# Performance work log

Hardware: AMD Instinct MI355X
Metric: run time of the kernel (lower is better)

## Reference

```python
import jax, jax.numpy as jnp
import numpy as np

N_HEAD = 16


def setup_inputs() -> dict:
    key = jax.random.key(0)
    k1, k2, k3 = jax.random.split(key, 3)
    B, S, D = 2, 2048, 1024
    return {
        "hidden_states": jax.random.normal(k1, (B, S, D), dtype=jnp.float32),
        "c_attn_w": jax.random.normal(k2, (D, 3 * D), dtype=jnp.float32) * 0.02,
        "c_attn_b": jnp.zeros((3 * D,), dtype=jnp.float32),
        "c_proj_w": jax.random.normal(k3, (D, D), dtype=jnp.float32) * 0.02,
        "c_proj_b": jnp.zeros((D,), dtype=jnp.float32),
    }


def reference(hidden_states, c_attn_w, c_attn_b, c_proj_w, c_proj_b):
    B, S, D = hidden_states.shape
    H = N_HEAD
    hd = D // H
    # Fused QKV projection (Conv1D == linear with transposed weight layout)
    qkv = hidden_states @ c_attn_w + c_attn_b  # [B,S,3D]
    q, k, v = jnp.split(qkv, 3, axis=-1)
    # split heads -> [B,H,S,hd]
    q = q.reshape(B, S, H, hd).transpose(0, 2, 1, 3)
    k = k.reshape(B, S, H, hd).transpose(0, 2, 1, 3)
    v = v.reshape(B, S, H, hd).transpose(0, 2, 1, 3)
    # scaled dot-product with causal mask
    scores = jnp.einsum("bhqd,bhkd->bhqk", q, k) / jnp.asarray(hd ** 0.5, q.dtype)
    causal = jnp.tril(jnp.ones((S, S), dtype=bool))  # [S,S]
    mask_value = jnp.finfo(scores.dtype).min
    scores = jnp.where(causal[None, None, :, :], scores, mask_value)
    attn_weights = jax.nn.softmax(scores, axis=-1)  # [B,H,S,S]
    ctx = jnp.einsum("bhqk,bhkd->bhqd", attn_weights, v)  # [B,H,S,hd]
    ctx = ctx.transpose(0, 2, 1, 3).reshape(B, S, D)  # merge heads
    out = ctx @ c_proj_w + c_proj_b  # [B,S,D]
    return out
```

## Files before the change

kernel.cpp:

```cpp
#include <hip/hip_runtime.h>
#include <hip/hip_bf16.h>

typedef __attribute__((ext_vector_type(8))) short short8;
typedef __attribute__((ext_vector_type(4))) float f32x4;
typedef __attribute__((ext_vector_type(16))) float f32x16;
typedef __attribute__((ext_vector_type(4))) unsigned short u16x4;
typedef __attribute__((ext_vector_type(8))) unsigned short u16x8;
typedef __attribute__((ext_vector_type(4))) unsigned int u32x4;

#define MFMA16(a, b, c) __builtin_amdgcn_mfma_f32_16x16x32_bf16((a), (b), (c), 0, 0, 0)
#define MFMA32(a, b, c) __builtin_amdgcn_mfma_f32_32x32x16_bf16((a), (b), (c), 0, 0, 0)

__device__ __forceinline__ unsigned short f2bf(float f) {
    union { float f; unsigned u; } v; v.f = f;
    return (unsigned short)((v.u + 0x7fffu + ((v.u >> 16) & 1u)) >> 16);
}

__device__ __forceinline__ float bf2f(unsigned short s) {
    union { unsigned u; float f; } v; v.u = (unsigned)s << 16;
    return v.f;
}

__device__ __forceinline__ unsigned cvtpk(float lo, float hi_) {
    unsigned r;
    asm volatile("v_cvt_pk_bf16_f32 %0, %1, %2" : "=v"(r) : "v"(lo), "v"(hi_));
    return r;
}

__global__ void cast_x_kernel(const float* __restrict__ x, ushort* __restrict__ y) {
    int i = blockIdx.x * blockDim.x + threadIdx.x;
    float4 v = ((const float4*)x)[i];
    u16x4 o = { f2bf(v.x), f2bf(v.y), f2bf(v.z), f2bf(v.w) };
    *(u16x4*)(y + (size_t)i * 4) = o;
}

__global__ void transpose_cast_kernel(const float* __restrict__ W, ushort* __restrict__ WT,
                                      int K, int N) {
    __shared__ ushort t[64][66];
    int n0 = blockIdx.x * 64, k0 = blockIdx.y * 64;
    int tn = threadIdx.x & 63, tg = threadIdx.x >> 6;
#pragma unroll
    for (int i = 0; i < 16; ++i) {
        int k = tg * 16 + i;
        t[tn][k] = f2bf(W[(size_t)(k0 + k) * N + n0 + tn]);
    }
    __syncthreads();
#pragma unroll
    for (int i = 0; i < 16; ++i) {
        int nn = tg * 16 + i;
        WT[(size_t)(n0 + nn) * K + k0 + tn] = t[nn][tn];
    }
}

#define QSCALE 0.18033688011112042f

template <int MODE>
__global__ __launch_bounds__(256, 3)
void gemm_bt_kernel(const ushort* __restrict__ A, const ushort* __restrict__ BT,
                    const float* __restrict__ bias,
                    ushort* __restrict__ Qb, ushort* __restrict__ Kb,
                    ushort* __restrict__ VT, float* __restrict__ Out,
                    int M, int N, int K) {
    __shared__ ushort Asm[3][128 * 32];
    __shared__ ushort Bsm[3][128 * 32];
    const int tid = threadIdx.x;
    const int lane = tid & 63;
    const int wv = tid >> 6;
    const int l15 = lane & 15, lg = lane >> 4;
    const int rm = (wv >> 1) * 64, cn = (wv & 1) * 64;
    const int row0 = blockIdx.y * 128, col0 = blockIdx.x * 128;

    const char* Agb = (const char*)(A + (size_t)row0 * K);
    const char* Bgb = (const char*)(BT + (size_t)col0 * K);
    const size_t rowbytes = (size_t)K * 2;

    f32x4 acc[4][4];
#pragma unroll
    for (int mi = 0; mi < 4; ++mi)
#pragma unroll
        for (int ni = 0; ni < 4; ++ni) acc[mi][ni] = f32x4{0.f, 0.f, 0.f, 0.f};

    const int sr0 = tid >> 2, sc0 = (tid & 3) ^ (sr0 & 3);
    const int sr1 = (tid + 256) >> 2, sc1 = (tid & 3) ^ (sr1 & 3);

#define GSTAGE(buf, k0_)                                                                \
    do {                                                                                \
        size_t kbyte = (size_t)(k0_)*2;                                                 \
        __builtin_amdgcn_global_load_lds(                                               \
            (const __attribute__((address_space(1))) void*)(Agb + (size_t)sr0 *         \
                rowbytes + kbyte + sc0 * 16),                                           \
            (__attribute__((address_space(3))) void*)((char*)&Asm[buf][0] + tid * 16),  \
            16, 0, 0);                                                                  \
        __builtin_amdgcn_global_load_lds(                                               \
            (const __attribute__((address_space(1))) void*)(Agb + (size_t)sr1 *         \
                rowbytes + kbyte + sc1 * 16),                                           \
            (__attribute__((address_space(3))) void*)((char*)&Asm[buf][0] + 4096 +      \
                tid * 16),                                                              \
            16, 0, 0);                                                                  \
        __builtin_amdgcn_global_load_lds(                                               \
            (const __attribute__((address_space(1))) void*)(Bgb + (size_t)sr0 *         \
                rowbytes + kbyte + sc0 * 16),                                           \
            (__attribute__((address_space(3))) void*)((char*)&Bsm[buf][0] + tid * 16),  \
            16, 0, 0);                                                                  \
        __builtin_amdgcn_global_load_lds(                                               \
            (const __attribute__((address_space(1))) void*)(Bgb + (size_t)sr1 *         \
                rowbytes + kbyte + sc1 * 16),                                           \
            (__attribute__((address_space(3))) void*)((char*)&Bsm[buf][0] + 4096 +      \
                tid * 16),                                                              \
            16, 0, 0);                                                                  \
    } while (0)

    const int NK = K >> 5;
    GSTAGE(0, 0);
    GSTAGE(1, 32);

    const int sw8 = (lg ^ (l15 & 3)) << 3;

    int cur = 0, stg = 2;
    for (int i = 0; i < NK; ++i) {
        if (i < NK - 1) asm volatile("s_waitcnt vmcnt(4)" ::: "memory");
        else            asm volatile("s_waitcnt vmcnt(0)" ::: "memory");
        __builtin_amdgcn_s_barrier();
        if (i + 2 < NK) GSTAGE(stg, (i + 2) * 32);
        short8 af[4], bf[4];
#pragma unroll
        for (int mi = 0; mi < 4; ++mi)
            af[mi] = *(const short8*)&Asm[cur][(rm + mi * 16 + l15) * 32 + sw8];
#pragma unroll
        for (int ni = 0; ni < 4; ++ni)
            bf[ni] = *(const short8*)&Bsm[cur][(cn + ni * 16 + l15) * 32 + sw8];
        __builtin_amdgcn_s_setprio(1);
#pragma unroll
        for (int mi = 0; mi < 4; ++mi)
#pragma unroll
            for (int ni = 0; ni < 4; ++ni)
                acc[mi][ni] = MFMA16(af[mi], bf[ni], acc[mi][ni]);
        __builtin_amdgcn_s_setprio(0);
        cur = (cur == 2) ? 0 : cur + 1;
        stg = (stg == 2) ? 0 : stg + 1;
    }
#undef GSTAGE

    if (MODE == 0) {
        const int sect = col0 >> 10;
#pragma unroll
        for (int ni = 0; ni < 4; ++ni) {
            int col = col0 + cn + ni * 16 + l15;
            float bv = bias[col];
            int dcol = col & 1023, h = dcol >> 6, dd = dcol & 63;
#pragma unroll
            for (int mi = 0; mi < 4; ++mi) {
                int mrow0 = row0 + rm + mi * 16 + lg * 4;
                if (sect == 2) {
                    int b = mrow0 >> 11, s = mrow0 & 2047;
                    u16x4 o;
#pragma unroll
                    for (int j = 0; j < 4; ++j) o[j] = f2bf(acc[mi][ni][j] + bv);
                    *(u16x4*)&VT[((size_t)((b << 4) + h) * 64 + dd) * 2048 + s] = o;
                } else {
                    ushort* dst = sect ? Kb : Qb;
                    float sc = sect ? 1.f : QSCALE;
#pragma unroll
                    for (int j = 0; j < 4; ++j) {
                        int tok = mrow0 + j;
                        int b = tok >> 11, s = tok & 2047;
                        dst[((size_t)((b << 4) + h) * 2048 + s) * 64 + dd] =
                            f2bf((acc[mi][ni][j] + bv) * sc);
                    }
                }
            }
        }
    } else {
#pragma unroll
        for (int ni = 0; ni < 4; ++ni) {
            int col = col0 + cn + ni * 16 + l15;
            float bv = bias[col];
#pragma unroll
            for (int mi = 0; mi < 4; ++mi) {
                int mrow0 = row0 + rm + mi * 16 + lg * 4;
#pragma unroll
                for (int j = 0; j < 4; ++j)
                    Out[(size_t)(mrow0 + j) * N + col] = acc[mi][ni][j] + bv;
            }
        }
    }
}

template <int SPLIT>
__global__ __launch_bounds__(256, 4)
void attn_kernel(const ushort* __restrict__ Qb, const ushort* __restrict__ Kb,
                 const ushort* __restrict__ VT, ushort* __restrict__ CTX,
                 ushort* __restrict__ OP, float* __restrict__ ML) {
    __shared__ __align__(16) ushort Ksm[2][64 * 64];
    __shared__ __align__(16) ushort Vsm[2][64 * 64];

    const int tid = threadIdx.x;
    const int lane = tid & 63;
    const int w = tid >> 6;
    const int l31 = lane & 31;
    const int hi = lane >> 5;
    const int r7 = l31 & 7;

    const int id = blockIdx.x;
    int bh, qt, half, cBeg, cEnd;
    if (SPLIT) {
        const int xcd = id & 7, jj = id >> 3;
        bh = (xcd << 2) + (jj & 3);
        const int r = jj >> 2;
        half = r >> 4;
        const int s = r & 15;
        qt = (s < 8) ? s : 23 - s;
        cBeg = half * (qt + 1);
        cEnd = cBeg + (qt + 1);
    } else {
        const int xcd = id & 7, jj = id >> 3;
        bh = (xcd << 2) + (jj >> 4);
        qt = ((jj >> 5) & 1) ? (jj & 15) : 15 - (jj & 15);
        half = 0; cBeg = 0; cEnd = 2 * qt + 2;
    }
    const int nc = 2 * qt + 2;
    const int qw0 = qt * 128 + w * 32;
    const int qrow = qw0 + l31;

    const ushort* Qh = Qb + (size_t)bh * 2048 * 64;
    const ushort* Kh = Kb + (size_t)bh * 2048 * 64;
    const ushort* Vh = VT + (size_t)bh * 64 * 2048;

    short8 qf[4];
#pragma unroll
    for (int dc = 0; dc < 4; ++dc)
        qf[dc] = *(const short8*)&Qh[(size_t)qrow * 64 + dc * 16 + hi * 8];

    const int srow = tid >> 3;
    const int sxor = ((tid & 7) ^ (srow & 7)) * 8;

#define GLL(src, dst) __builtin_amdgcn_global_load_lds(                                 \
        (const __attribute__((address_space(1))) void*)(src),                           \
        (__attribute__((address_space(3))) void*)(dst), 16, 0, 0)

#define STAGE(buf, kb_)                                                                 \
    do {                                                                                \
        const ushort* kp = Kh + (size_t)((kb_) + srow) * 64 + sxor;                     \
        GLL(kp, (char*)&Ksm[buf][0] + tid * 16);                                        \
        GLL(kp + 32 * 64, (char*)&Ksm[buf][0] + 4096 + tid * 16);                       \
        const ushort* vp = Vh + (size_t)srow * 2048 + (kb_) + sxor;                     \
        GLL(vp, (char*)&Vsm[buf][0] + tid * 16);                                        \
        GLL(vp + (size_t)32 * 2048, (char*)&Vsm[buf][0] + 4096 + tid * 16);             \
    } while (0)

    const int cdiag = 2 * qt + (w >> 1);

    STAGE(0, cBeg * 64);
    __syncthreads();

    float mrun = -1e30f, lsum = 0.f;
    f32x16 acc0, acc1;
#pragma unroll
    for (int r = 0; r < 16; ++r) { acc0[r] = 0.f; acc1[r] = 0.f; }

    int cur = 0;
    for (int c = cBeg; c < cEnd; ++c) {
        const int kb = c * 64;
        if (c + 1 < cEnd) STAGE(cur ^ 1, kb + 64);

        if (!(w < 2 && c == nc - 1)) {
            const ushort* Kc = &Ksm[cur][0];
            const ushort* Vc = &Vsm[cur][0];

            f32x16 st0, st1;
#pragma unroll
            for (int r = 0; r < 16; ++r) { st0[r] = 0.f; st1[r] = 0.f; }
            __builtin_amdgcn_s_setprio(1);
#pragma unroll
            for (int dc = 0; dc < 4; ++dc) {
                short8 kf0 = *(const short8*)(Kc + l31 * 64 + (((dc * 2 + hi) ^ r7) << 3));
                short8 kf1 = *(const short8*)(Kc + (32 + l31) * 64 + (((dc * 2 + hi) ^ r7) << 3));
                st0 = MFMA32(kf0, qf[dc], st0);
                st1 = MFMA32(kf1, qf[dc], st1);
            }
            __builtin_amdgcn_s_setprio(0);

            if (c == cdiag) {
                const int base0 = kb + (hi << 2);
                const int base1 = kb + 32 + (hi << 2);
#pragma unroll
                for (int r = 0; r < 16; ++r) {
                    int k0 = base0 + ((r & 3) + 8 * (r >> 2));
                    int k1 = base1 + ((r & 3) + 8 * (r >> 2));
                    st0[r] = (k0 <= qrow) ? st0[r] : -1e30f;
                    st1[r] = (k1 <= qrow) ? st1[r] : -1e30f;
                }
            }

            float tm[8];
#pragma unroll
            for (int i = 0; i < 8; ++i)
                tm[i] = fmaxf(fmaxf(st0[i], st0[i + 8]), fmaxf(st1[i], st1[i + 8]));
            float tmax = fmaxf(fmaxf(fmaxf(tm[0], tm[1]), fmaxf(tm[2], tm[3])),
                               fmaxf(fmaxf(tm[4], tm[5]), fmaxf(tm[6], tm[7])));
            tmax = fmaxf(tmax, __shfl_xor(tmax, 32));

            if (!__all(tmax <= mrun + 8.0f)) {
                float mnew = fmaxf(mrun, tmax);
                float sc = exp2f(mrun - mnew);
#pragma unroll
                for (int r = 0; r < 16; ++r) { acc0[r] *= sc; acc1[r] *= sc; }
                lsum *= sc;
                mrun = mnew;
            }

#pragma unroll
            for (int r = 0; r < 16; ++r) st0[r] = exp2f(st0[r] - mrun);
#pragma unroll
            for (int r = 0; r < 16; ++r) st1[r] = exp2f(st1[r] - mrun);
            float ts[8];
#pragma unroll
            for (int i = 0; i < 8; ++i) ts[i] = st0[i] + st0[i + 8];
#pragma unroll
            for (int i = 0; i < 8; ++i) ts[i] += st1[i] + st1[i + 8];
            float tsum = ((ts[0] + ts[1]) + (ts[2] + ts[3])) +
                         ((ts[4] + ts[5]) + (ts[6] + ts[7]));
            lsum += tsum;

#define MAKE_PFRAG(st, kcL, out)                                                        \
    do {                                                                                \
        unsigned a0 = cvtpk(st[8 * kcL + 0], st[8 * kcL + 1]);                          \
        unsigned a1 = cvtpk(st[8 * kcL + 2], st[8 * kcL + 3]);                          \
        unsigned b0 = cvtpk(st[8 * kcL + 4], st[8 * kcL + 5]);                          \
        unsigned b1 = cvtpk(st[8 * kcL + 6], st[8 * kcL + 7]);                          \
        asm volatile("v_permlane32_swap_b32 %0, %1" : "+v"(a0), "+v"(b0));              \
        asm volatile("v_permlane32_swap_b32 %0, %1" : "+v"(a1), "+v"(b1));              \
        u32x4 fw;                                                                       \
        fw.x = a0; fw.y = a1; fw.z = b0; fw.w = b1;                                     \
        out = __builtin_bit_cast(short8, fw);                                           \
    } while (0)

#define PV_GROUP(st, kcL, g)                                                            \
    do {                                                                                \
        short8 pf;                                                                      \
        MAKE_PFRAG(st, kcL, pf);                                                        \
        short8 v0 = *(const short8*)(Vc + l31 * 64 + (((2 * (g) + hi) ^ r7) << 3));     \
        short8 v1 = *(const short8*)(Vc + (32 + l31) * 64 +                             \
                                     (((2 * (g) + hi) ^ r7) << 3));                     \
        acc0 = MFMA32(v0, pf, acc0);                                                    \
        acc1 = MFMA32(v1, pf, acc1);                                                    \
    } while (0)

            __builtin_amdgcn_s_setprio(1);
            PV_GROUP(st0, 0, 0);
            PV_GROUP(st0, 1, 1);
            PV_GROUP(st1, 0, 2);
            PV_GROUP(st1, 1, 3);
            __builtin_amdgcn_s_setprio(0);
#undef PV_GROUP
#undef MAKE_PFRAG
        }

        __syncthreads();
        cur ^= 1;
    }
#undef STAGE
#undef GLL

    lsum += __shfl_xor(lsum, 32);

    if (SPLIT) {
        const int pidx = ((bh << 4) + qt) * 2 + half;
        ushort* op = OP + (size_t)pidx * 8192 + (size_t)(w * 32 + l31) * 64;
#define WRITE_PART(accv, dt)                                                            \
    do {                                                                                \
        _Pragma("unroll")                                                               \
        for (int q2 = 0; q2 < 4; ++q2) {                                                \
            int d0 = dt * 32 + 8 * q2 + (hi << 2);                                      \
            u16x4 o;                                                                    \
            _Pragma("unroll")                                                           \
            for (int j = 0; j < 4; ++j) o[j] = f2bf(accv[4 * q2 + j]);                  \
            *(u16x4*)&op[d0] = o;                                                       \
        }                                                                               \
    } while (0)
        WRITE_PART(acc0, 0);
        WRITE_PART(acc1, 1);
#undef WRITE_PART
        if (hi == 0) {
            float2 r2 = { mrun, lsum };
            *(float2*)&ML[((size_t)pidx * 128 + w * 32 + l31) * 2] = r2;
        }
    } else {
        const float inv = 1.f / lsum;
        const int b = bh >> 4, h = bh & 15;
        const size_t tokrow = ((size_t)b * 2048 + qw0 + l31) * 1024 + (size_t)h * 64;
#define WRITE_DT(accv, dt)                                                              \
    do {                                                                                \
        _Pragma("unroll")                                                               \
        for (int q2 = 0; q2 < 4; ++q2) {                                                \
            int d0 = dt * 32 + 8 * q2 + (hi << 2);                                      \
            u16x4 o;                                                                    \
            _Pragma("unroll")                                                           \
            for (int j = 0; j < 4; ++j) o[j] = f2bf(accv[4 * q2 + j] * inv);            \
            *(u16x4*)&CTX[tokrow + d0] = o;                                             \
        }                                                                               \
    } while (0)
        WRITE_DT(acc0, 0);
        WRITE_DT(acc1, 1);
#undef WRITE_DT
    }
}

__global__ __launch_bounds__(256)
void merge_kernel(const ushort* __restrict__ OP, const float* __restrict__ ML,
                  ushort* __restrict__ CTX) {
    const int bid = blockIdx.x;
    const int bh = bid >> 4, qt = bid & 15;
    const int tid = threadIdx.x;
    const size_t base0 = (size_t)(bid * 2) * 8192;
    const size_t mlb = (size_t)(bid * 2) * 128;
#pragma unroll
    for (int it = 0; it < 4; ++it) {
        const int g = tid + it * 256;
        const int row = g >> 3, d0 = (g & 7) * 8;
        const float2 ml0 = *(const float2*)&ML[(mlb + row) * 2];
        const float2 ml1 = *(const float2*)&ML[(mlb + 128 + row) * 2];
        const float M = fmaxf(ml0.x, ml1.x);
        const float f0 = exp2f(ml0.x - M), f1 = exp2f(ml1.x - M);
        const float inv = 1.f / (f0 * ml0.y + f1 * ml1.y);
        const u16x8 a0 = *(const u16x8*)&OP[base0 + (size_t)g * 8];
        const u16x8 a1 = *(const u16x8*)&OP[base0 + 8192 + (size_t)g * 8];
        u16x8 o;
#pragma unroll
        for (int j = 0; j < 8; ++j)
            o[j] = f2bf((f0 * bf2f(a0[j]) + f1 * bf2f(a1[j])) * inv);
        const size_t tok = (size_t)(bh >> 4) * 2048 + qt * 128 + row;
        *(u16x8*)&CTX[tok * 1024 + (size_t)(bh & 15) * 64 + d0] = o;
    }
}

extern "C" void kernel_launch(void* const* d_in, const int* in_sizes, int n_in,
                              void* d_out, int out_size, void* d_ws, size_t ws_size,
                              hipStream_t stream) {
    const float* X     = (const float*)d_in[0];
    const float* Wqkv  = (const float*)d_in[1];
    const float* bqkv  = (const float*)d_in[2];
    const float* Wproj = (const float*)d_in[3];
    const float* bproj = (const float*)d_in[4];
    float* Out = (float*)d_out;

    ushort* Xb     = (ushort*)d_ws;
    ushort* WqkvT  = Xb + (size_t)4096 * 1024;
    ushort* WprojT = WqkvT + (size_t)3072 * 1024;
    ushort* Qb     = WprojT + (size_t)1024 * 1024;
    ushort* Kb     = Qb + (size_t)4096 * 1024;
    ushort* VT     = Kb + (size_t)4096 * 1024;
    ushort* CTX    = VT + (size_t)4096 * 1024;
    ushort* OP = (ushort*)((char*)d_ws + (size_t)48 * 1024 * 1024);
    float*  ML = (float*)(OP + (size_t)1024 * 128 * 64);
    const size_t NEED = (size_t)(48 + 16 + 1) * 1024 * 1024;

    cast_x_kernel<<<4096, 256, 0, stream>>>(X, Xb);
    transpose_cast_kernel<<<dim3(48, 16), 256, 0, stream>>>(Wqkv, WqkvT, 1024, 3072);
    transpose_cast_kernel<<<dim3(16, 16), 256, 0, stream>>>(Wproj, WprojT, 1024, 1024);
    gemm_bt_kernel<0><<<dim3(24, 32), 256, 0, stream>>>(Xb, WqkvT, bqkv, Qb, Kb, VT, nullptr,
                                                        4096, 3072, 1024);
    if (ws_size >= NEED) {
        attn_kernel<1><<<1024, 256, 0, stream>>>(Qb, Kb, VT, CTX, OP, ML);
        merge_kernel<<<512, 256, 0, stream>>>(OP, ML, CTX);
    } else {
        attn_kernel<0><<<512, 256, 0, stream>>>(Qb, Kb, VT, CTX, nullptr, nullptr);
    }
    gemm_bt_kernel<1><<<dim3(8, 32), 256, 0, stream>>>(CTX, WprojT, bproj, nullptr, nullptr,
                                                       nullptr, Out, 4096, 1024, 1024);
}
```

Measured before the change: 124.7 us.

## Fuse split-KV merge into attention via atomic counter and merge prep kernels

The three cast/transpose kernels become one prep kernel that dispatches on block index, which saves launches. The separate merge kernel is removed. Each split-attention block now writes its partial result, fences, and bumps a per-tile atomic counter, and whichever half finishes second reads the other half's partial and writes the merged context directly. This drops a kernel launch and a re-read of both partials, at the cost of a hipMemsetAsync to clear the flags and extra fences and syncs at the end of attention.

```diff
diff --git a/kernel.cpp b/kernel.cpp
--- a/kernel.cpp
+++ b/kernel.cpp
@@ -27,18 +27,26 @@
     return r;
 }
 
-__global__ void cast_x_kernel(const float* __restrict__ x, ushort* __restrict__ y) {
-    int i = blockIdx.x * blockDim.x + threadIdx.x;
-    float4 v = ((const float4*)x)[i];
-    u16x4 o = { f2bf(v.x), f2bf(v.y), f2bf(v.z), f2bf(v.w) };
-    *(u16x4*)(y + (size_t)i * 4) = o;
-}
-
-__global__ void transpose_cast_kernel(const float* __restrict__ W, ushort* __restrict__ WT,
-                                      int K, int N) {
+__global__ __launch_bounds__(256)
+void prep_kernel(const float* __restrict__ X, ushort* __restrict__ Xb,
+                 const float* __restrict__ Wqkv, ushort* __restrict__ WqkvT,
+                 const float* __restrict__ Wproj, ushort* __restrict__ WprojT) {
     __shared__ ushort t[64][66];
-    int n0 = blockIdx.x * 64, k0 = blockIdx.y * 64;
-    int tn = threadIdx.x & 63, tg = threadIdx.x >> 6;
+    const int b = blockIdx.x;
+    const int tid = threadIdx.x;
+    if (b < 4096) {
+        int i = b * 256 + tid;
+        float4 v = ((const float4*)X)[i];
+        u16x4 o = { f2bf(v.x), f2bf(v.y), f2bf(v.z), f2bf(v.w) };
+        *(u16x4*)(Xb + (size_t)i * 4) = o;
+        return;
+    }
+    const float* W; ushort* WT; int N, idx;
+    if (b < 4864) { W = Wqkv;  WT = WqkvT;  N = 3072; idx = b - 4096; }
+    else          { W = Wproj; WT = WprojT; N = 1024; idx = b - 4864; }
+    const int nblk = N >> 6;
+    const int n0 = (idx % nblk) * 64, k0 = (idx / nblk) * 64;
+    const int tn = tid & 63, tg = tid >> 6;
 #pragma unroll
     for (int i = 0; i < 16; ++i) {
         int k = tg * 16 + i;
@@ -48,7 +56,7 @@
 #pragma unroll
     for (int i = 0; i < 16; ++i) {
         int nn = tg * 16 + i;
-        WT[(size_t)(n0 + nn) * K + k0 + tn] = t[nn][tn];
+        WT[(size_t)(n0 + nn) * 1024 + k0 + tn] = t[nn][tn];
     }
 }
 
@@ -190,9 +198,11 @@
 __global__ __launch_bounds__(256, 4)
 void attn_kernel(const ushort* __restrict__ Qb, const ushort* __restrict__ Kb,
                  const ushort* __restrict__ VT, ushort* __restrict__ CTX,
-                 ushort* __restrict__ OP, float* __restrict__ ML) {
+                 ushort* __restrict__ OP, float* __restrict__ ML,
+                 int* __restrict__ FLAG) {
     __shared__ __align__(16) ushort Ksm[2][64 * 64];
     __shared__ __align__(16) ushort Vsm[2][64 * 64];
+    __shared__ int sOld;
 
     const int tid = threadIdx.x;
     const int lane = tid & 63;
@@ -365,7 +375,9 @@
     lsum += __shfl_xor(lsum, 32);
 
     if (SPLIT) {
-        const int pidx = ((bh << 4) + qt) * 2 + half;
+        const int bid = (bh << 4) + qt;
+        const int pidx = bid * 2 + half;
+        const int podx = bid * 2 + (1 - half);
         ushort* op = OP + (size_t)pidx * 8192 + (size_t)(w * 32 + l31) * 64;
 #define WRITE_PART(accv, dt)                                                            \
     do {                                                                                \
@@ -385,6 +397,36 @@
             float2 r2 = { mrun, lsum };
             *(float2*)&ML[((size_t)pidx * 128 + w * 32 + l31) * 2] = r2;
         }
+        __threadfence();
+        __syncthreads();
+        if (tid == 0) sOld = atomicAdd(&FLAG[bid], 1);
+        __syncthreads();
+        if (sOld == 1) {
+            __threadfence();
+            const float2 mlo = *(const float2*)&ML[((size_t)podx * 128 + w * 32 + l31) * 2];
+            const float M = fmaxf(mrun, mlo.x);
+            const float fw_ = exp2f(mrun - M), fl_ = exp2f(mlo.x - M);
+            const float inv = 1.f / (fw_ * lsum + fl_ * mlo.y);
+            const ushort* opo = OP + (size_t)podx * 8192 + (size_t)(w * 32 + l31) * 64;
+            const int b = bh >> 4, h = bh & 15;
+            const size_t tokrow = ((size_t)b * 2048 + qw0 + l31) * 1024 + (size_t)h * 64;
+#define WRITE_MERGED(accv, dt)                                                          \
+    do {                                                                                \
+        _Pragma("unroll")                                                               \
+        for (int q2 = 0; q2 < 4; ++q2) {                                                \
+            int d0 = dt * 32 + 8 * q2 + (hi << 2);                                      \
+            u16x4 ao = *(const u16x4*)&opo[d0];                                         \
+            u16x4 o;                                                                    \
+            _Pragma("unroll")                                                           \
+            for (int j = 0; j < 4; ++j)                                                 \
+                o[j] = f2bf((fw_ * accv[4 * q2 + j] + fl_ * bf2f(ao[j])) * inv);        \
+            *(u16x4*)&CTX[tokrow + d0] = o;                                             \
+        }                                                                               \
+    } while (0)
+            WRITE_MERGED(acc0, 0);
+            WRITE_MERGED(acc1, 1);
+#undef WRITE_MERGED
+        }
     } else {
         const float inv = 1.f / lsum;
         const int b = bh >> 4, h = bh & 15;
@@ -403,34 +445,6 @@
         WRITE_DT(acc0, 0);
         WRITE_DT(acc1, 1);
 #undef WRITE_DT
-    }
-}
-
-__global__ __launch_bounds__(256)
-void merge_kernel(const ushort* __restrict__ OP, const float* __restrict__ ML,
-                  ushort* __restrict__ CTX) {
-    const int bid = blockIdx.x;
-    const int bh = bid >> 4, qt = bid & 15;
-    const int tid = threadIdx.x;
-    const size_t base0 = (size_t)(bid * 2) * 8192;
-    const size_t mlb = (size_t)(bid * 2) * 128;
-#pragma unroll
-    for (int it = 0; it < 4; ++it) {
-        const int g = tid + it * 256;
-        const int row = g >> 3, d0 = (g & 7) * 8;
-        const float2 ml0 = *(const float2*)&ML[(mlb + row) * 2];
-        const float2 ml1 = *(const float2*)&ML[(mlb + 128 + row) * 2];
-        const float M = fmaxf(ml0.x, ml1.x);
-        const float f0 = exp2f(ml0.x - M), f1 = exp2f(ml1.x - M);
-        const float inv = 1.f / (f0 * ml0.y + f1 * ml1.y);
-        const u16x8 a0 = *(const u16x8*)&OP[base0 + (size_t)g * 8];
-        const u16x8 a1 = *(const u16x8*)&OP[base0 + 8192 + (size_t)g * 8];
-        u16x8 o;
-#pragma unroll
-        for (int j = 0; j < 8; ++j)
-            o[j] = f2bf((f0 * bf2f(a0[j]) + f1 * bf2f(a1[j])) * inv);
-        const size_t tok = (size_t)(bh >> 4) * 2048 + qt * 128 + row;
-        *(u16x8*)&CTX[tok * 1024 + (size_t)(bh & 15) * 64 + d0] = o;
     }
 }
 
@@ -453,18 +467,17 @@
     ushort* CTX    = VT + (size_t)4096 * 1024;
     ushort* OP = (ushort*)((char*)d_ws + (size_t)48 * 1024 * 1024);
     float*  ML = (float*)(OP + (size_t)1024 * 128 * 64);
-    const size_t NEED = (size_t)(48 + 16 + 1) * 1024 * 1024;
-
-    cast_x_kernel<<<4096, 256, 0, stream>>>(X, Xb);
-    transpose_cast_kernel<<<dim3(48, 16), 256, 0, stream>>>(Wqkv, WqkvT, 1024, 3072);
-    transpose_cast_kernel<<<dim3(16, 16), 256, 0, stream>>>(Wproj, WprojT, 1024, 1024);
+    int*  FLAG = (int*)(ML + (size_t)1024 * 128 * 2);
+    const size_t NEED = (size_t)(48 + 16 + 1) * 1024 * 1024 + 4096;
+
+    prep_kernel<<<5120, 256, 0, stream>>>(X, Xb, Wqkv, WqkvT, Wproj, WprojT);
     gemm_bt_kernel<0><<<dim3(24, 32), 256, 0, stream>>>(Xb, WqkvT, bqkv, Qb, Kb, VT, nullptr,
                                                         4096, 3072, 1024);
     if (ws_size >= NEED) {
-        attn_kernel<1><<<1024, 256, 0, stream>>>(Qb, Kb, VT, CTX, OP, ML);
-        merge_kernel<<<512, 256, 0, stream>>>(OP, ML, CTX);
+        hipMemsetAsync(FLAG, 0, 512 * sizeof(int), stream);
+        attn_kernel<1><<<1024, 256, 0, stream>>>(Qb, Kb, VT, CTX, OP, ML, FLAG);
     } else {
-        attn_kernel<0><<<512, 256, 0, stream>>>(Qb, Kb, VT, CTX, nullptr, nullptr);
+        attn_kernel<0><<<512, 256, 0, stream>>>(Qb, Kb, VT, CTX, nullptr, nullptr, nullptr);
     }
     gemm_bt_kernel<1><<<dim3(8, 32), 256, 0, stream>>>(CTX, WprojT, bproj, nullptr, nullptr,
                                                        nullptr, Out, 4096, 1024, 1024);
```

Measured after the change: 324.8 us. +160.4%, slower.
